# Optimization experiments

Measured on AMD Instinct MI355X. Metric: run time of the kernel, lower is better.

## Reference

```python
import jax, jax.numpy as jnp
import numpy as np

N_NODES = 100000
N_EDGES = 3200000
IN_DIM, HID_DIM, LAT_DIM = 6, 32, 16


def gcn_conv(x, src, dst, W, b, num_nodes):
    """PyG-style GCNConv: add self-loops, symmetric deg^{-1/2} norm, linear, scatter-add.
    src/dst already include self-loops."""
    h = x @ W  # [N, out_dim] -- transform before propagate (small dims)
    ones = jnp.ones(src.shape[0], dtype=x.dtype)
    deg = jax.ops.segment_sum(ones, dst, num_segments=num_nodes)  # in-degree incl. self-loop
    dinv = jax.lax.rsqrt(jnp.maximum(deg, 1.0))
    norm = dinv[src] * dinv[dst]  # [E]
    msg = h[src] * norm[:, None]  # [E, out_dim] -- dominant memory traffic
    out = jax.ops.segment_sum(msg, dst, num_segments=num_nodes)
    return out + b


def setup_inputs() -> dict:
    key = jax.random.key(0)
    k1, k2, k3, k4 = jax.random.split(key, 4)
    x = jax.random.normal(k1, (N_NODES, IN_DIM), dtype=jnp.float32)
    edge_index = jax.random.randint(k2, (2, N_EDGES), 0, N_NODES, dtype=jnp.int64)
    # Glorot-ish init for weights, zeros for biases (PyG GCNConv defaults)
    W1 = jax.random.normal(k3, (IN_DIM, HID_DIM), dtype=jnp.float32) / np.sqrt(IN_DIM)
    b1 = jnp.zeros((HID_DIM,), dtype=jnp.float32)
    W2 = jax.random.normal(k4, (HID_DIM, LAT_DIM), dtype=jnp.float32) / np.sqrt(HID_DIM)
    b2 = jnp.zeros((LAT_DIM,), dtype=jnp.float32)
    return {"x": x, "edge_index": edge_index, "W1": W1, "b1": b1, "W2": W2, "b2": b2}


def reference(x, edge_index, W1, b1, W2, b2):
    num_nodes = x.shape[0]
    loops = jnp.arange(num_nodes, dtype=edge_index.dtype)
    src = jnp.concatenate([edge_index[0], loops])
    dst = jnp.concatenate([edge_index[1], loops])
    h = gcn_conv(x, src, dst, W1, b1, num_nodes)
    h = jax.nn.relu(h)
    # dropout is identity in eval mode (reference baseline)
    z = gcn_conv(h, src, dst, W2, b2, num_nodes)
    return z
```

## Files before the change

kernel.cpp:

```cpp
#include <hip/hip_runtime.h>
#include <hip/hip_fp16.h>

#define N_NODES 100000
#define N_EDGES 3200000
#define IN_DIM 6
#define HID_DIM 32
#define LAT_DIM 16

#define NPB 128
#define NB 782
#define CAP 4800
#define AB_BLOCKS 512
#define CH ((N_EDGES + AB_BLOCKS - 1) / AB_BLOCKS)
#define PL_T 512
#define LP_CAP 2080

__global__ void k_init(int* __restrict__ bcur) {
    int i = blockIdx.x * blockDim.x + threadIdx.x;
    if (i < NB) bcur[i] = i * CAP;
}

__global__ void __launch_bounds__(PL_T) k_bplace(const int* __restrict__ src,
                                                 const int* __restrict__ dst,
                                                 int* __restrict__ bcur,
                                                 int* __restrict__ bedge, int E) {
    __shared__ int hist[NB];
    __shared__ int lbase[NB];
    __shared__ int gbase[NB];
    __shared__ int cur[NB];
    __shared__ int part[PL_T];
    __shared__ int stage[CH];
    __shared__ unsigned short sbkt[CH];
    int t = threadIdx.x;
    for (int i = t; i < NB; i += PL_T) { hist[i] = 0; cur[i] = 0; }
    __syncthreads();
    int beg = blockIdx.x * CH, end = min(beg + CH, E);
    for (int e = beg + t; e < end; e += PL_T)
        atomicAdd(&hist[dst[e] >> 7], 1);
    __syncthreads();
    int i0 = 2 * t;
    int a = (i0 < NB) ? hist[i0] : 0;
    int b = (i0 + 1 < NB) ? hist[i0 + 1] : 0;
    part[t] = a + b;
    __syncthreads();
    for (int off = 1; off < PL_T; off <<= 1) {
        int v = (t >= off) ? part[t - off] : 0;
        __syncthreads();
        part[t] += v;
        __syncthreads();
    }
    int ex = (t == 0) ? 0 : part[t - 1];
    if (i0 < NB) lbase[i0] = ex;
    if (i0 + 1 < NB) lbase[i0 + 1] = ex + a;
    __syncthreads();
    for (int i = t; i < NB; i += PL_T)
        gbase[i] = hist[i] ? atomicAdd(&bcur[i], hist[i]) : 0;
    __syncthreads();
    for (int e = beg + t; e < end; e += PL_T) {
        int d = dst[e];
        int s = __builtin_nontemporal_load(src + e);
        int bkt = d >> 7;
        int r = atomicAdd(&cur[bkt], 1);
        int pos = lbase[bkt] + r;
        stage[pos] = (s << 7) | (d & (NPB - 1));
        sbkt[pos] = (unsigned short)bkt;
    }
    __syncthreads();
    int total = end - beg;
    for (int j = t; j < total; j += PL_T) {
        int bkt = sbkt[j];
        __builtin_nontemporal_store(stage[j], bedge + gbase[bkt] + (j - lbase[bkt]));
    }
}

__global__ void __launch_bounds__(256) k_sort(const int* __restrict__ bcur,
                                              const int* __restrict__ bedge,
                                              const float* __restrict__ x,
                                              int2* __restrict__ rowse,
                                              int* __restrict__ perm,
                                              float* __restrict__ dinv,
                                              __half* __restrict__ xs, int N) {
    int b = blockIdx.x;
    __shared__ int cnt[NPB], base[NPB], cur[NPB], scn[NPB];
    __shared__ float dvs[NPB];
    __shared__ int pstage[CAP];
    int t = threadIdx.x;
    if (t < NPB) cnt[t] = 0;
    __syncthreads();
    int beg = b * CAP, end = bcur[b];
    int m = end - beg;
    for (int k = t; k < m; k += blockDim.x)
        atomicAdd(&cnt[bedge[beg + k] & (NPB - 1)], 1);
    __syncthreads();
    if (t < NPB) scn[t] = cnt[t];
    __syncthreads();
    for (int off = 1; off < NPB; off <<= 1) {
        int v = 0;
        if (t < NPB && t >= off) v = scn[t - off];
        __syncthreads();
        if (t < NPB) scn[t] += v;
        __syncthreads();
    }
    if (t < NPB) {
        int ex = scn[t] - cnt[t];
        base[t] = ex;
        cur[t] = 0;
        int node = (b << 7) + t;
        if (node < N) {
            float dv = rsqrtf((float)(cnt[t] + 1));
            dvs[t] = dv;
            dinv[node] = dv;
            rowse[node] = make_int2(beg + ex, beg + ex + cnt[t]);
        }
    }
    __syncthreads();
    for (int k = t; k < m; k += blockDim.x) {
        int w = bedge[beg + k];
        int dl = w & (NPB - 1);
        int pos = base[dl] + atomicAdd(&cur[dl], 1);
        pstage[pos] = w >> 7;
    }
    __syncthreads();
    for (int k = t; k < m; k += blockDim.x)
        __builtin_nontemporal_store(pstage[k], perm + beg + k);
    for (int i = t; i < NPB * 4; i += blockDim.x) {
        int nl = i >> 2, d2 = (i & 3) * 2;
        int node = (b << 7) + nl;
        if (node < N) {
            float dv = dvs[nl];
            float v0 = (d2 < IN_DIM) ? x[(size_t)node * IN_DIM + d2] * dv : 0.f;
            float v1 = (d2 + 1 < IN_DIM) ? x[(size_t)node * IN_DIM + d2 + 1] * dv : 0.f;
            *(__half2*)(xs + (size_t)node * 8 + d2) = __floats2half2_rn(v0, v1);
        }
    }
}

__global__ void __launch_bounds__(256) k_agg1f(const int2* __restrict__ rowse,
                                               const int* __restrict__ perm,
                                               const __half* __restrict__ xs,
                                               const float* __restrict__ dinv,
                                               const float* __restrict__ b1,
                                               const float* __restrict__ W1,
                                               const float* __restrict__ W2,
                                               __half* __restrict__ h2s) {
    __shared__ float w1[IN_DIM * HID_DIM];
    __shared__ float w2[HID_DIM * LAT_DIM];
    __shared__ float bsh[HID_DIM];
    __shared__ float ash[32][HID_DIM + 1];
    __shared__ float y[32][8];
    __shared__ int lperm[LP_CAP];
    int t = threadIdx.x;
    for (int i = t; i < IN_DIM * HID_DIM; i += 256) w1[i] = W1[i];
    for (int i = t; i < HID_DIM * LAT_DIM; i += 256) w2[i] = W2[i];
    if (t < HID_DIM) bsh[t] = b1[t];
    int nl = t >> 3, p = t & 7;
    int n0 = blockIdx.x * 32;
    int node = n0 + nl;
    int gbeg = rowse[n0].x;
    int gend = rowse[n0 + 31].y;
    int m = gend - gbeg;
    int2 se = rowse[node];
    float acc = 0.f;
    if (m <= LP_CAP) {
        for (int i = t; i < m; i += 256) lperm[i] = __builtin_nontemporal_load(perm + gbeg + i);
        __syncthreads();
        int k = se.x - gbeg, lend = se.y - gbeg;
        for (; k + 16 <= lend; k += 16) {
            int ss[16];
#pragma unroll
            for (int j = 0; j < 16; j++) ss[j] = lperm[k + j];
            __half gg[16];
#pragma unroll
            for (int j = 0; j < 16; j++) gg[j] = xs[(size_t)ss[j] * 8 + p];
            float part = 0.f;
#pragma unroll
            for (int j = 0; j < 16; j++) part += __half2float(gg[j]);
            acc += part;
        }
        for (; k < lend; ++k) acc += __half2float(xs[(size_t)lperm[k] * 8 + p]);
    } else {
        __syncthreads();
        for (int k = se.x; k < se.y; ++k)
            acc += __half2float(xs[(size_t)perm[k] * 8 + p]);
    }
    acc += __half2float(xs[(size_t)node * 8 + p]);
    y[nl][p] = acc;
    __syncthreads();
    float dv = dinv[node];
    {
        float yy[IN_DIM];
#pragma unroll
        for (int k = 0; k < IN_DIM; k++) yy[k] = y[nl][k];
        int c0 = p * 4;
#pragma unroll
        for (int q = 0; q < 4; q++) {
            float z = 0.f;
#pragma unroll
            for (int k = 0; k < IN_DIM; k++) z += yy[k] * w1[k * HID_DIM + c0 + q];
            ash[nl][c0 + q] = fmaxf(dv * z + bsh[c0 + q], 0.f);
        }
    }
    __syncthreads();
    {
        int c = p * 2;
        float z0 = 0.f, z1 = 0.f;
#pragma unroll
        for (int k = 0; k < HID_DIM; k++) {
            float a = ash[nl][k];
            z0 += a * w2[k * LAT_DIM + c];
            z1 += a * w2[k * LAT_DIM + c + 1];
        }
        __half2 h = __floats2half2_rn(dv * z0, dv * z1);
        *(__half2*)(h2s + (size_t)node * LAT_DIM + c) = h;
    }
}

__global__ void __launch_bounds__(256) k_agg2(const int2* __restrict__ rowse,
                                              const int* __restrict__ perm,
                                              const __half* __restrict__ h2s,
                                              const float* __restrict__ dinv,
                                              const float* __restrict__ b2,
                                              float* __restrict__ out) {
    __shared__ int lperm[LP_CAP];
    int t = threadIdx.x;
    int n0 = blockIdx.x * 32;
    int node = n0 + (t >> 3), p = t & 7;
    int gbeg = rowse[n0].x;
    int gend = rowse[n0 + 31].y;
    int m = gend - gbeg;
    int2 se = rowse[node];
    float2 acc = make_float2(0.f, 0.f);
    if (m <= LP_CAP) {
        for (int i = t; i < m; i += 256) lperm[i] = __builtin_nontemporal_load(perm + gbeg + i);
        __syncthreads();
        int k = se.x - gbeg, lend = se.y - gbeg;
        for (; k + 16 <= lend; k += 16) {
            int ss[16];
#pragma unroll
            for (int j = 0; j < 16; j++) ss[j] = lperm[k + j];
            __half2 gg[16];
#pragma unroll
            for (int j = 0; j < 16; j++)
                gg[j] = *(const __half2*)(h2s + (size_t)ss[j] * LAT_DIM + p * 2);
            float px = 0.f, py = 0.f;
#pragma unroll
            for (int j = 0; j < 16; j++) {
                float2 f = __half22float2(gg[j]);
                px += f.x; py += f.y;
            }
            acc.x += px; acc.y += py;
        }
        for (; k < lend; ++k) {
            float2 f = __half22float2(*(const __half2*)(h2s + (size_t)lperm[k] * LAT_DIM + p * 2));
            acc.x += f.x; acc.y += f.y;
        }
    } else {
        __syncthreads();
        for (int k = se.x; k < se.y; ++k) {
            float2 f = __half22float2(*(const __half2*)(h2s + (size_t)perm[k] * LAT_DIM + p * 2));
            acc.x += f.x; acc.y += f.y;
        }
    }
    float2 hs = __half22float2(*(const __half2*)(h2s + (size_t)node * LAT_DIM + p * 2));
    float dv = dinv[node];
    float2 bb = *(const float2*)(b2 + p * 2);
    float2 o;
    o.x = dv * (acc.x + hs.x) + bb.x;
    o.y = dv * (acc.y + hs.y) + bb.y;
    *(float2*)(out + (size_t)node * LAT_DIM + p * 2) = o;
}

extern "C" void kernel_launch(void* const* d_in, const int* in_sizes, int n_in,
                              void* d_out, int out_size, void* d_ws, size_t ws_size,
                              hipStream_t stream) {
    const float* x  = (const float*)d_in[0];
    const int*   ei = (const int*)d_in[1];
    const float* W1 = (const float*)d_in[2];
    const float* b1 = (const float*)d_in[3];
    const float* W2 = (const float*)d_in[4];
    const float* b2 = (const float*)d_in[5];
    float* out = (float*)d_out;

    const int N = N_NODES, E = N_EDGES;
    const int* src = ei;
    const int* dst = ei + E;

    char* ws = (char*)d_ws;
    size_t off = 0;
    auto take = [&](size_t bytes) -> void* {
        void* p = ws + off;
        off += (bytes + 255) & ~(size_t)255;
        return p;
    };
    int*    bcur  = (int*)take((size_t)NB * 4);
    int*    bedge = (int*)take((size_t)NB * CAP * 4);
    int*    perm  = (int*)take((size_t)NB * CAP * 4);
    int2*   rowse = (int2*)take((size_t)N * 8);
    float*  dinv  = (float*)take((size_t)N * 4);
    __half* xs    = (__half*)take((size_t)N * 8 * 2);
    __half* h2s   = (__half*)take((size_t)N * LAT_DIM * 2);

    const int B = 256;
    k_init<<<(NB + B - 1) / B, B, 0, stream>>>(bcur);
    k_bplace<<<AB_BLOCKS, PL_T, 0, stream>>>(src, dst, bcur, bedge, E);
    k_sort<<<NB, B, 0, stream>>>(bcur, bedge, x, rowse, perm, dinv, xs, N);
    k_agg1f<<<N / 32, B, 0, stream>>>(rowse, perm, xs, dinv, b1, W1, W2, h2s);
    k_agg2<<<N / 32, B, 0, stream>>>(rowse, perm, h2s, dinv, b2, out);
}
```

Before: 114.2 us.

## Widen layer-2 gather to 8-byte loads with 64 nodes per block; drop nontemporal hints

The second aggregation kernel now gives each thread four latent features through 8-byte gathers, so 4 threads cover a node and a block handles 64 nodes. The edge-list tile and its shared-memory cap grow to match, and partial last blocks are bounded. Separately, the nontemporal stores and loads on bedge and perm become ordinary accesses, so these intermediates may stay in cache for the kernels that read them next. The wider gathers cut the number of load instructions per edge, but each thread now walks the same edge list with half as many threads per node.

```diff
diff --git a/kernel.cpp b/kernel.cpp
--- a/kernel.cpp
+++ b/kernel.cpp
@@ -14,6 +14,7 @@
 #define CH ((N_EDGES + AB_BLOCKS - 1) / AB_BLOCKS)
 #define PL_T 512
 #define LP_CAP 2080
+#define LP2_CAP 2560
 
 __global__ void k_init(int* __restrict__ bcur) {
     int i = blockIdx.x * blockDim.x + threadIdx.x;
@@ -69,7 +70,7 @@
     int total = end - beg;
     for (int j = t; j < total; j += PL_T) {
         int bkt = sbkt[j];
-        __builtin_nontemporal_store(stage[j], bedge + gbase[bkt] + (j - lbase[bkt]));
+        bedge[gbase[bkt] + (j - lbase[bkt])] = stage[j];
     }
 }
 
@@ -122,7 +123,7 @@
     }
     __syncthreads();
     for (int k = t; k < m; k += blockDim.x)
-        __builtin_nontemporal_store(pstage[k], perm + beg + k);
+        perm[beg + k] = pstage[k];
     for (int i = t; i < NPB * 4; i += blockDim.x) {
         int nl = i >> 2, d2 = (i & 3) * 2;
         int node = (b << 7) + nl;
@@ -162,7 +163,7 @@
     int2 se = rowse[node];
     float acc = 0.f;
     if (m <= LP_CAP) {
-        for (int i = t; i < m; i += 256) lperm[i] = __builtin_nontemporal_load(perm + gbeg + i);
+        for (int i = t; i < m; i += 256) lperm[i] = perm[gbeg + i];
         __syncthreads();
         int k = se.x - gbeg, lend = se.y - gbeg;
         for (; k + 16 <= lend; k += 16) {
@@ -220,54 +221,64 @@
                                               const __half* __restrict__ h2s,
                                               const float* __restrict__ dinv,
                                               const float* __restrict__ b2,
-                                              float* __restrict__ out) {
-    __shared__ int lperm[LP_CAP];
+                                              float* __restrict__ out, int N) {
+    __shared__ int lperm[LP2_CAP];
     int t = threadIdx.x;
-    int n0 = blockIdx.x * 32;
-    int node = n0 + (t >> 3), p = t & 7;
+    int n0 = blockIdx.x * 64;
+    int node = n0 + (t >> 2), p = t & 3;
+    int nlast = min(n0 + 63, N - 1);
     int gbeg = rowse[n0].x;
-    int gend = rowse[n0 + 31].y;
+    int gend = rowse[nlast].y;
     int m = gend - gbeg;
-    int2 se = rowse[node];
-    float2 acc = make_float2(0.f, 0.f);
-    if (m <= LP_CAP) {
-        for (int i = t; i < m; i += 256) lperm[i] = __builtin_nontemporal_load(perm + gbeg + i);
+    int2 se = (node <= nlast) ? rowse[node] : make_int2(gbeg, gbeg);
+    float4 acc = make_float4(0.f, 0.f, 0.f, 0.f);
+    if (m <= LP2_CAP) {
+        for (int i = t; i < m; i += 256) lperm[i] = perm[gbeg + i];
         __syncthreads();
         int k = se.x - gbeg, lend = se.y - gbeg;
         for (; k + 16 <= lend; k += 16) {
             int ss[16];
 #pragma unroll
             for (int j = 0; j < 16; j++) ss[j] = lperm[k + j];
-            __half2 gg[16];
+            uint2 gg[16];
 #pragma unroll
             for (int j = 0; j < 16; j++)
-                gg[j] = *(const __half2*)(h2s + (size_t)ss[j] * LAT_DIM + p * 2);
-            float px = 0.f, py = 0.f;
+                gg[j] = *(const uint2*)(h2s + (size_t)ss[j] * LAT_DIM + p * 4);
 #pragma unroll
             for (int j = 0; j < 16; j++) {
-                float2 f = __half22float2(gg[j]);
-                px += f.x; py += f.y;
+                float2 f0 = __half22float2(*(const __half2*)&gg[j].x);
+                float2 f1 = __half22float2(*(const __half2*)&gg[j].y);
+                acc.x += f0.x; acc.y += f0.y; acc.z += f1.x; acc.w += f1.y;
             }
-            acc.x += px; acc.y += py;
         }
         for (; k < lend; ++k) {
-            float2 f = __half22float2(*(const __half2*)(h2s + (size_t)lperm[k] * LAT_DIM + p * 2));
-            acc.x += f.x; acc.y += f.y;
+            uint2 g = *(const uint2*)(h2s + (size_t)lperm[k] * LAT_DIM + p * 4);
+            float2 f0 = __half22float2(*(const __half2*)&g.x);
+            float2 f1 = __half22float2(*(const __half2*)&g.y);
+            acc.x += f0.x; acc.y += f0.y; acc.z += f1.x; acc.w += f1.y;
         }
     } else {
         __syncthreads();
         for (int k = se.x; k < se.y; ++k) {
-            float2 f = __half22float2(*(const __half2*)(h2s + (size_t)perm[k] * LAT_DIM + p * 2));
-            acc.x += f.x; acc.y += f.y;
-        }
-    }
-    float2 hs = __half22float2(*(const __half2*)(h2s + (size_t)node * LAT_DIM + p * 2));
-    float dv = dinv[node];
-    float2 bb = *(const float2*)(b2 + p * 2);
-    float2 o;
-    o.x = dv * (acc.x + hs.x) + bb.x;
-    o.y = dv * (acc.y + hs.y) + bb.y;
-    *(float2*)(out + (size_t)node * LAT_DIM + p * 2) = o;
+            uint2 g = *(const uint2*)(h2s + (size_t)perm[k] * LAT_DIM + p * 4);
+            float2 f0 = __half22float2(*(const __half2*)&g.x);
+            float2 f1 = __half22float2(*(const __half2*)&g.y);
+            acc.x += f0.x; acc.y += f0.y; acc.z += f1.x; acc.w += f1.y;
+        }
+    }
+    if (node < N) {
+        uint2 hh = *(const uint2*)(h2s + (size_t)node * LAT_DIM + p * 4);
+        float2 h0 = __half22float2(*(const __half2*)&hh.x);
+        float2 h1 = __half22float2(*(const __half2*)&hh.y);
+        float dv = dinv[node];
+        float4 bb = *(const float4*)(b2 + p * 4);
+        float4 o;
+        o.x = dv * (acc.x + h0.x) + bb.x;
+        o.y = dv * (acc.y + h0.y) + bb.y;
+        o.z = dv * (acc.z + h1.x) + bb.z;
+        o.w = dv * (acc.w + h1.y) + bb.w;
+        *(float4*)(out + (size_t)node * LAT_DIM + p * 4) = o;
+    }
 }
 
 extern "C" void kernel_launch(void* const* d_in, const int* in_sizes, int n_in,
@@ -305,5 +316,5 @@
     k_bplace<<<AB_BLOCKS, PL_T, 0, stream>>>(src, dst, bcur, bedge, E);
     k_sort<<<NB, B, 0, stream>>>(bcur, bedge, x, rowse, perm, dinv, xs, N);
     k_agg1f<<<N / 32, B, 0, stream>>>(rowse, perm, xs, dinv, b1, W1, W2, h2s);
-    k_agg2<<<N / 32, B, 0, stream>>>(rowse, perm, h2s, dinv, b2, out);
-}
+    k_agg2<<<(N + 63) / 64, B, 0, stream>>>(rowse, perm, h2s, dinv, b2, out, N);
+}
```

Result: faster. 107.5 us (-5.9%).
